# Kernel optimization log

Hardware: AMD Instinct MI355X
Metric: run time of the kernel (lower is better)

Reference implementation:

```python
import jax, jax.numpy as jnp
import numpy as np

VOCAB = 30000  # opts.numofingr
EPS = 1e-12


def setup_inputs() -> dict:
    key = jax.random.key(0)
    ks = jax.random.split(key, 8)
    B, L = 4096, 20
    ingrs = jax.random.randint(ks[0], (B, L), 0, VOCAB, dtype=jnp.int32)
    lengths = jax.random.randint(ks[1], (B,), 0, 21, dtype=jnp.int32)
    # MLP params: Linear(VOCAB,512) -> ReLU -> Linear(512,1024) -> ReLU -> Linear(1024,2047)
    # Stored so that one-hot @ W1 == W1[ingr]; i.e. W1 has shape [VOCAB, 512].
    W1 = jax.random.normal(ks[2], (VOCAB, 512), dtype=jnp.float32) * (1.0 / np.sqrt(VOCAB))
    b1 = jax.random.normal(ks[3], (512,), dtype=jnp.float32) * 0.01
    W2 = jax.random.normal(ks[4], (512, 1024), dtype=jnp.float32) * (1.0 / np.sqrt(512))
    b2 = jax.random.normal(ks[5], (1024,), dtype=jnp.float32) * 0.01
    W3 = jax.random.normal(ks[6], (1024, 2047), dtype=jnp.float32) * (1.0 / np.sqrt(1024))
    b3 = jax.random.normal(ks[7], (2047,), dtype=jnp.float32) * 0.01
    return {"ingrs": ingrs, "lengths": lengths,
            "W1": W1, "b1": b1, "W2": W2, "b2": b2, "W3": W3, "b3": b3}


def reference(ingrs, lengths, W1, b1, W2, b2, W3, b3):
    # One-hot x MLP first layer == embedding row gather: [B, L, 512]
    h1 = jax.nn.relu(W1[ingrs] + b1)
    h2 = jax.nn.relu(jnp.einsum('blh,hk->blk', h1, W2) + b2)   # [B, L, 1024]
    emb = jnp.einsum('blk,ko->blo', h2, W3) + b3               # [B, L, 2047]
    # L2-normalize each ingredient embedding (torch norm(p=2, dim=1) on [1,2047])
    nrm = jnp.sqrt(jnp.sum(emb * emb, axis=-1, keepdims=True))
    emb = emb / jnp.maximum(nrm, EPS)
    # Masked sum over valid ingredients (ingr_ln truncation in the source)
    L = ingrs.shape[1]
    mask = (jnp.arange(L)[None, :] < lengths[:, None]).astype(emb.dtype)  # [B, L]
    return jnp.einsum('blo,bl->bo', emb, mask)                 # [B, 2047]
```

## Files before the change

### kernel.cpp

```cpp
#include <hip/hip_runtime.h>

#define VOCAB 30000
#define MPAD  30080
#define MT_PAD 240

typedef __attribute__((ext_vector_type(8))) short bf16x8;
typedef __attribute__((ext_vector_type(4))) float f32x4;

__device__ __forceinline__ unsigned short f2bf(float f) {
    unsigned int u = __builtin_bit_cast(unsigned int, f);
    u += 0x7fffu + ((u >> 16) & 1u);
    return (unsigned short)(u >> 16);
}
__device__ __forceinline__ float bf2f(unsigned int h) {
    unsigned int u = h << 16;
    return __builtin_bit_cast(float, u);
}

__device__ __forceinline__ void async16(const void* g, void* l) {
    __builtin_amdgcn_global_load_lds(
        (__attribute__((address_space(1))) void*)g,
        (__attribute__((address_space(3))) void*)l, 16, 0, 0);
}

__global__ void k_mark(const int* __restrict__ ingrs, const int* __restrict__ lengths,
                       int* __restrict__ flags, int* __restrict__ cnt)
{
    const int i = blockIdx.x * 256 + threadIdx.x;
    if (i == 0) *cnt = 0;
    if (i >= 4096 * 20) return;
    const int b = i / 20;
    const int l = i - b * 20;
    if (l < lengths[b]) flags[ingrs[i]] = 1;
}

__global__ void k_assign(const int* __restrict__ flags, int* __restrict__ remap,
                         int* __restrict__ cnt)
{
    const int i = blockIdx.x * 256 + threadIdx.x;
    if (i < VOCAB && flags[i] == 1) remap[i] = atomicAdd(cnt, 1);
}


__device__ __forceinline__ void transpose_body(
    const float* __restrict__ in, unsigned short* __restrict__ out,
    int K, int Nin, int n0, int k0, int tid, float (*t)[65])
{
#pragma unroll
    for (int p = 0; p < 16; ++p) {
        const int lin = p * 256 + tid;
        const int kk = lin >> 6, nn = lin & 63;
        const int n = n0 + nn;
        t[kk][nn] = (n < Nin) ? in[(size_t)(k0 + kk) * Nin + n] : 0.f;
    }
    __syncthreads();
#pragma unroll
    for (int p = 0; p < 16; ++p) {
        const int lin = p * 256 + tid;
        const int nn = lin >> 6, kk = lin & 63;
        out[(size_t)(n0 + nn) * K + k0 + kk] = f2bf(t[kk][nn]);
    }
}

__device__ __forceinline__ void gemm_body(
    unsigned short* smem,
    const unsigned short* __restrict__ A, const unsigned short* __restrict__ BT,
    const float* __restrict__ bias, int bias_n, unsigned short* __restrict__ C,
    int K, int N, int relu, int mc, int id, int nt_shift)
{
    const int w  = id >> 3;
    const int n_tile = w & ((1 << nt_shift) - 1);
    const int m_tile = (id & 7) + ((w >> nt_shift) << 3);
    const int m0 = m_tile * 128;
    if (m0 >= mc) return;
    const int n0 = n_tile * 128;

    unsigned short* As = smem;
    unsigned short* Bs = smem + 8192;

    const int tid  = threadIdx.x;
    const int lane = tid & 63;
    const int wid  = tid >> 6;
    const int wr   = wid >> 1;
    const int wc   = wid & 1;
    const int q  = lane >> 4;
    const int ml = lane & 15;

    f32x4 acc[4][4];
    const f32x4 zero = {0.f, 0.f, 0.f, 0.f};
#pragma unroll
    for (int i = 0; i < 4; ++i)
#pragma unroll
        for (int j = 0; j < 4; ++j) acc[i][j] = zero;

    const int rg = lane >> 3;
    const int kc = (lane & 7) ^ rg;
    const unsigned short* pA = A  + (size_t)(m0 + wid * 32 + rg) * K + kc * 8;
    const unsigned short* pB = BT + (size_t)(n0 + wid * 32 + rg) * K + kc * 8;
    unsigned short* lA = &As[wid * 4 * 512 + lane * 8];
    unsigned short* lB = &Bs[wid * 4 * 512 + lane * 8];

    const int swz0 = (q ^ (ml & 7)) * 8;

    for (int k0 = 0; k0 < K; k0 += 64) {
#pragma unroll
        for (int gg = 0; gg < 4; ++gg) {
            async16(pA + (size_t)gg * 8 * K, lA + gg * 512);
            async16(pB + (size_t)gg * 8 * K, lB + gg * 512);
        }
        pA += 64; pB += 64;
        __syncthreads();

        bf16x8 af[4], bfr[4];
#pragma unroll
        for (int t = 0; t < 4; ++t) {
            af[t]  = *(const bf16x8*)&As[(wr * 64 + t * 16 + ml) * 64 + swz0];
            bfr[t] = *(const bf16x8*)&Bs[(wc * 64 + t * 16 + ml) * 64 + swz0];
        }
#pragma unroll
        for (int i = 0; i < 4; ++i)
#pragma unroll
            for (int j = 0; j < 4; ++j)
                acc[i][j] = __builtin_amdgcn_mfma_f32_16x16x32_bf16(
                    af[i], bfr[j], acc[i][j], 0, 0, 0);
#pragma unroll
        for (int t = 0; t < 4; ++t) {
            af[t]  = *(const bf16x8*)&As[(wr * 64 + t * 16 + ml) * 64 + (swz0 ^ 32)];
            bfr[t] = *(const bf16x8*)&Bs[(wc * 64 + t * 16 + ml) * 64 + (swz0 ^ 32)];
        }
#pragma unroll
        for (int i = 0; i < 4; ++i)
#pragma unroll
            for (int j = 0; j < 4; ++j)
                acc[i][j] = __builtin_amdgcn_mfma_f32_16x16x32_bf16(
                    af[i], bfr[j], acc[i][j], 0, 0, 0);

        __syncthreads();
    }

#pragma unroll
    for (int i = 0; i < 4; ++i) {
#pragma unroll
        for (int j = 0; j < 4; ++j) {
#pragma unroll
            for (int r = 0; r < 4; ++r) {
                const int rl = wr * 64 + i * 16 + q * 4 + r;
                const int cl = wc * 64 + j * 16 + ml;
                float v = acc[i][j][r];
                const int col = n0 + cl;
                v += (col < bias_n) ? bias[col] : 0.f;
                if (relu) v = fmaxf(v, 0.f);
                smem[rl * 136 + cl] = f2bf(v);
            }
        }
    }
    __syncthreads();
#pragma unroll
    for (int p = 0; p < 8; ++p) {
        const int rr = p * 16 + (tid >> 4);
        const int cc = tid & 15;
        const uint4 val = *(const uint4*)&smem[rr * 136 + cc * 8];
        *(uint4*)&C[(size_t)(m0 + rr) * N + n0 + cc * 8] = val;
    }
}

__global__ __launch_bounds__(256)
void k_prep(const float* __restrict__ W1, const float* __restrict__ b1,
            const int* __restrict__ flags, const int* __restrict__ remap,
            unsigned short* __restrict__ A1,
            const float* __restrict__ W2, unsigned short* __restrict__ W2T)
{
    __shared__ float t[64][65];
    const int bid = blockIdx.x;
    const int tid = threadIdx.x;

    if (bid < 15000) {
        const int id = bid * 2 + (tid >> 7);
        if (flags[id] != 1) return;
        const int row = remap[id];
        const int k4  = (tid & 127) * 4;
        const float4 w  = *(const float4*)(W1 + (size_t)id * 512 + k4);
        const float4 bb = *(const float4*)(b1 + k4);
        unsigned short o[4];
        o[0] = f2bf(fmaxf(w.x + bb.x, 0.f));
        o[1] = f2bf(fmaxf(w.y + bb.y, 0.f));
        o[2] = f2bf(fmaxf(w.z + bb.z, 0.f));
        o[3] = f2bf(fmaxf(w.w + bb.w, 0.f));
        *(uint2*)(A1 + (size_t)row * 512 + k4) = *(const uint2*)o;
    } else {
        const int local = bid - 15000;
        transpose_body(W2, W2T, 512, 1024, (local & 15) * 64, (local >> 4) * 64, tid, t);
    }
}

__global__ __launch_bounds__(256)
void k_gemm1(const unsigned short* __restrict__ A1, const unsigned short* __restrict__ W2T,
             const float* __restrict__ b2, unsigned short* __restrict__ H2,
             const int* __restrict__ cnt,
             const float* __restrict__ W3, unsigned short* __restrict__ W3T,
             const int* __restrict__ ingrs, const int* __restrict__ lengths,
             const int* __restrict__ remap, int* __restrict__ slots)
{
    __shared__ __align__(16) unsigned short smem[128 * 136];
    const int bid = blockIdx.x;
    if (bid < MT_PAD * 8) {
        const int mc = (*cnt + 127) & ~127;
        gemm_body(smem, A1, W2T, b2, 1024, H2, 512, 1024, 1, mc, bid, 3);
    } else if (bid < MT_PAD * 8 + 512) {
        const int local = bid - MT_PAD * 8;
        transpose_body(W3, W3T, 1024, 2047, (local & 31) * 64, (local >> 5) * 64,
                       threadIdx.x, (float(*)[65])smem);
    } else {
        const int i = (bid - (MT_PAD * 8 + 512)) * 256 + threadIdx.x;
        if (i < 4096 * 20) {
            const int b = i / 20;
            const int l = i - b * 20;
            if (l < lengths[b]) slots[i] = remap[ingrs[i]];
        }
    }
}

__global__ __launch_bounds__(256)
void k_gemm2(const unsigned short* __restrict__ H2, const unsigned short* __restrict__ W3T,
             const float* __restrict__ b3, unsigned short* __restrict__ Table,
             const int* __restrict__ cnt)
{
    __shared__ __align__(16) unsigned short smem[128 * 136];
    const int mc = (*cnt + 127) & ~127;
    gemm_body(smem, H2, W3T, b3, 2047, Table, 1024, 2048, 0, mc, blockIdx.x, 4);
}

__global__ __launch_bounds__(64)
void k_gather(const int* __restrict__ lengths, const int* __restrict__ slots,
              const unsigned short* __restrict__ Table, float* __restrict__ out)
{
    const int b    = blockIdx.x;
    const int lane = threadIdx.x;

    float acc[32];
#pragma unroll
    for (int j = 0; j < 32; ++j) acc[j] = 0.f;

    const int len = lengths[b];
    if (len > 0) {
        uint4 u[4];
        {
            const int slot = slots[b * 20];
            const uint4* rp = (const uint4*)(Table + (size_t)slot * 2048);
#pragma unroll
            for (int c = 0; c < 4; ++c) u[c] = rp[c * 64 + lane];
        }
        for (int l = 0; l < len; ++l) {
            uint4 cu[4];
#pragma unroll
            for (int c = 0; c < 4; ++c) cu[c] = u[c];
            if (l + 1 < len) {
                const int ns = slots[b * 20 + l + 1];
                const uint4* rp = (const uint4*)(Table + (size_t)ns * 2048);
#pragma unroll
                for (int c = 0; c < 4; ++c) u[c] = rp[c * 64 + lane];
            }
            float v[32];
#pragma unroll
            for (int c = 0; c < 4; ++c) {
                v[c*8+0] = bf2f(cu[c].x & 0xffffu); v[c*8+1] = bf2f(cu[c].x >> 16);
                v[c*8+2] = bf2f(cu[c].y & 0xffffu); v[c*8+3] = bf2f(cu[c].y >> 16);
                v[c*8+4] = bf2f(cu[c].z & 0xffffu); v[c*8+5] = bf2f(cu[c].z >> 16);
                v[c*8+6] = bf2f(cu[c].w & 0xffffu); v[c*8+7] = bf2f(cu[c].w >> 16);
            }
            float s = 0.f;
#pragma unroll
            for (int j = 0; j < 32; ++j) s += v[j] * v[j];
#pragma unroll
            for (int off = 1; off < 64; off <<= 1) s += __shfl_xor(s, off, 64);
            const float invn = 1.0f / fmaxf(sqrtf(s), 1e-12f);
#pragma unroll
            for (int j = 0; j < 32; ++j) acc[j] += v[j] * invn;
        }
    }

    const size_t base = (size_t)b * 2047;
#pragma unroll
    for (int c = 0; c < 4; ++c) {
        const int col = (c * 64 + lane) * 8;
#pragma unroll
        for (int j = 0; j < 8; ++j)
            if (col + j < 2047) out[base + col + j] = acc[c * 8 + j];
    }
}


extern "C" void kernel_launch(void* const* d_in, const int* in_sizes, int n_in,
                              void* d_out, int out_size, void* d_ws, size_t ws_size,
                              hipStream_t stream)
{
    const int*   ingrs   = (const int*)d_in[0];
    const int*   lengths = (const int*)d_in[1];
    const float* W1 = (const float*)d_in[2];
    const float* b1 = (const float*)d_in[3];
    const float* W2 = (const float*)d_in[4];
    const float* b2 = (const float*)d_in[5];
    const float* W3 = (const float*)d_in[6];
    const float* b3 = (const float*)d_in[7];
    float* out = (float*)d_out;

    char* ws = (char*)d_ws;
    unsigned short* A1    = (unsigned short*)(ws);
    unsigned short* H2    = (unsigned short*)(ws + 30801920);
    unsigned short* Table = (unsigned short*)(ws + 92405760);
    unsigned short* W2T   = (unsigned short*)(ws + 215613440);
    unsigned short* W3T   = (unsigned short*)(ws + 216662016);
    int*            flags = (int*)(ws + 220856320);
    int*            remap = (int*)(ws + 220976320);
    int*            cnt   = (int*)(ws + 221096320);
    int*            slots = (int*)(ws + 221216448);

    k_mark  <<<(4096 * 20 + 255) / 256, 256, 0, stream>>>(ingrs, lengths, flags, cnt);
    k_assign<<<(VOCAB + 255) / 256, 256, 0, stream>>>(flags, remap, cnt);
    k_prep<<<15128, 256, 0, stream>>>(W1, b1, flags, remap, A1, W2, W2T);
    k_gemm1<<<MT_PAD * 8 + 512 + 320, 256, 0, stream>>>(
        A1, W2T, b2, H2, cnt, W3, W3T, ingrs, lengths, remap, slots);
    k_gemm2<<<MT_PAD * 16, 256, 0, stream>>>(H2, W3T, b3, Table, cnt);

    k_gather<<<4096, 64, 0, stream>>>(lengths, slots, Table, out);
}
```

Baseline: 328.3 us.

## Rewrite second GEMM as 256x256-tile, 512-thread, double-buffered async-LDS MFMA kernel

Replaces the shared 128x128 gemm_body call for the H2·W3 layer with a dedicated kernel. It uses 256x256 output tiles, 8 waves, and double-buffered global_load_lds staging with an XOR-swizzled LDS layout. MFMA phases are interleaved with barriers and priority hints, and the epilogue goes through LDS so global stores are coalesced. The aim is more data reuse per tile and less load latency exposed in the dominant GEMM. The cost is 128KB of LDS per block and heavy register use, which limits occupancy, plus a coarser padding of the M dimension to multiples of 256.

```diff
diff --git a/kernel.cpp b/kernel.cpp
--- a/kernel.cpp
+++ b/kernel.cpp
@@ -220,14 +220,149 @@
     }
 }
 
-__global__ __launch_bounds__(256)
-void k_gemm2(const unsigned short* __restrict__ H2, const unsigned short* __restrict__ W3T,
-             const float* __restrict__ b3, unsigned short* __restrict__ Table,
+#define G2_NK 16
+#define G2_K  1024
+#define G2_N  2048
+#define G2_MT 120
+
+#define MF(a, b, c) __builtin_amdgcn_mfma_f32_16x16x32_bf16(a, b, c, 0, 0, 0)
+
+__global__ __launch_bounds__(512, 2)
+void k_gemm2(const unsigned short* __restrict__ A, const unsigned short* __restrict__ BT,
+             const float* __restrict__ bias, unsigned short* __restrict__ C,
              const int* __restrict__ cnt)
 {
-    __shared__ __align__(16) unsigned short smem[128 * 136];
-    const int mc = (*cnt + 127) & ~127;
-    gemm_body(smem, H2, W3T, b3, 2047, Table, 1024, 2048, 0, mc, blockIdx.x, 4);
+    __shared__ __align__(16) unsigned short lds[65536];
+
+    const int id = blockIdx.x;
+    const int w  = id >> 3;
+    const int n_tile = w & 7;
+    const int m_tile = (id & 7) + ((w >> 3) << 3);
+    const int m0 = m_tile * 256;
+    const int mc = (*cnt + 255) & ~255;
+    if (m0 >= mc) return;
+    const int n0 = n_tile * 256;
+
+    const int tid  = threadIdx.x;
+    const int lane = tid & 63;
+    const int w0   = tid >> 6;
+    const int wr   = w0 >> 2;
+    const int wc   = w0 & 3;
+    const int q    = lane >> 4;
+    const int ml   = lane & 15;
+    const int m7   = ml & 7;
+
+    f32x4 acc[8][4];
+    const f32x4 zero = {0.f, 0.f, 0.f, 0.f};
+#pragma unroll
+    for (int i = 0; i < 8; ++i)
+#pragma unroll
+        for (int j = 0; j < 4; ++j) acc[i][j] = zero;
+
+    const int rg = lane >> 3;
+    const int kc = (lane & 7) ^ rg;
+    const unsigned short* pA0 = A  + (size_t)(m0 + w0 * 32 + rg) * G2_K + kc * 8;
+    const unsigned short* pB0 = BT + (size_t)(n0 + w0 * 32 + rg) * G2_K + kc * 8;
+    const int dstoff = w0 * 2048 + lane * 8;
+
+#define G2_STAGE(BUF, KT) do {                                             \
+        const unsigned short* _sa = pA0 + (size_t)(KT) * 64;               \
+        const unsigned short* _sb = pB0 + (size_t)(KT) * 64;               \
+        unsigned short* _da = &lds[(BUF) * 16384 + dstoff];                \
+        unsigned short* _db = &lds[32768 + (BUF) * 16384 + dstoff];        \
+        _Pragma("unroll")                                                  \
+        for (int g = 0; g < 4; ++g) {                                      \
+            async16(_sa + (size_t)g * 8 * G2_K, _da + g * 512);            \
+            async16(_sb + (size_t)g * 8 * G2_K, _db + g * 512);            \
+        }                                                                  \
+    } while (0)
+
+#define LDA(I, S) (*(const bf16x8*)&lds[cb + ((wr * 128 + (I) * 16 + ml) * 64) + ((((S) * 4 + q) ^ m7) * 8)])
+#define LDB(J, S) (*(const bf16x8*)&lds[32768 + cb + ((wc * 64 + (J) * 16 + ml) * 64) + ((((S) * 4 + q) ^ m7) * 8)])
+
+#define G2_PHASE(I0) do {                                                  \
+        bf16x8 a00 = LDA(I0, 0), a01 = LDA(I0, 1);                         \
+        bf16x8 a10 = LDA(I0 + 1, 0), a11 = LDA(I0 + 1, 1);                 \
+        __builtin_amdgcn_s_barrier();                                      \
+        asm volatile("s_waitcnt lgkmcnt(0)" ::: "memory");                 \
+        __builtin_amdgcn_sched_barrier(0);                                 \
+        __builtin_amdgcn_s_setprio(1);                                     \
+        _Pragma("unroll")                                                  \
+        for (int j = 0; j < 4; ++j) acc[I0][j]     = MF(a00, bfr[0][j], acc[I0][j]);     \
+        _Pragma("unroll")                                                  \
+        for (int j = 0; j < 4; ++j) acc[I0 + 1][j] = MF(a10, bfr[0][j], acc[I0 + 1][j]); \
+        _Pragma("unroll")                                                  \
+        for (int j = 0; j < 4; ++j) acc[I0][j]     = MF(a01, bfr[1][j], acc[I0][j]);     \
+        _Pragma("unroll")                                                  \
+        for (int j = 0; j < 4; ++j) acc[I0 + 1][j] = MF(a11, bfr[1][j], acc[I0 + 1][j]); \
+        __builtin_amdgcn_s_setprio(0);                                     \
+        __builtin_amdgcn_s_barrier();                                      \
+    } while (0)
+
+    G2_STAGE(0, 0);
+    G2_STAGE(1, 1);
+    asm volatile("s_waitcnt vmcnt(8)" ::: "memory");
+    __builtin_amdgcn_s_barrier();
+
+    for (int t = 0; t < G2_NK; ++t) {
+        const int cb = (t & 1) * 16384;
+
+        bf16x8 bfr[2][4];
+#pragma unroll
+        for (int s = 0; s < 2; ++s)
+#pragma unroll
+            for (int j = 0; j < 4; ++j) bfr[s][j] = LDB(j, s);
+
+        G2_PHASE(0);
+        G2_PHASE(2);
+        G2_PHASE(4);
+        G2_PHASE(6);
+
+        if (t + 2 < G2_NK) {
+            G2_STAGE(t & 1, t + 2);
+            asm volatile("s_waitcnt vmcnt(8)" ::: "memory");
+        } else {
+            asm volatile("s_waitcnt vmcnt(0)" ::: "memory");
+        }
+        __builtin_amdgcn_s_barrier();
+    }
+
+#undef G2_PHASE
+#undef LDA
+#undef LDB
+#undef G2_STAGE
+
+    float bv[4];
+#pragma unroll
+    for (int j = 0; j < 4; ++j) {
+        const int col = n0 + wc * 64 + j * 16 + ml;
+        bv[j] = (col < 2047) ? bias[col] : 0.f;
+    }
+    for (int h = 0; h < 2; ++h) {
+        if (wr == h) {
+#pragma unroll
+            for (int i = 0; i < 8; ++i)
+#pragma unroll
+                for (int j = 0; j < 4; ++j)
+#pragma unroll
+                    for (int r = 0; r < 4; ++r) {
+                        const float v = acc[i][j][r] + bv[j];
+                        lds[(i * 16 + q * 4 + r) * 280 + wc * 64 + j * 16 + ml] = f2bf(v);
+                    }
+        }
+        __syncthreads();
+#pragma unroll
+        for (int p = 0; p < 8; ++p) {
+            const int row  = p * 16 + (tid >> 5);
+            const int c8   = (tid & 31) * 8;
+            const int grow = m0 + h * 128 + row;
+            if (grow < MPAD) {
+                *(uint4*)&C[(size_t)grow * G2_N + n0 + c8] =
+                    *(const uint4*)&lds[row * 280 + c8];
+            }
+        }
+        __syncthreads();
+    }
 }
 
 __global__ __launch_bounds__(64)
@@ -320,7 +455,7 @@
     k_prep<<<15128, 256, 0, stream>>>(W1, b1, flags, remap, A1, W2, W2T);
     k_gemm1<<<MT_PAD * 8 + 512 + 320, 256, 0, stream>>>(
         A1, W2T, b2, H2, cnt, W3, W3T, ingrs, lengths, remap, slots);
-    k_gemm2<<<MT_PAD * 16, 256, 0, stream>>>(H2, W3T, b3, Table, cnt);
+    k_gemm2<<<G2_MT * 8, 512, 0, stream>>>(H2, W3T, b3, Table, cnt);
 
     k_gather<<<4096, 64, 0, stream>>>(lengths, slots, Table, out);
 }
```

Measured after the change: 320.5 us. 2.4% less time.
